# Optimization experiments

Hardware: AMD Instinct MI355X
Metric: run time of the kernel (lower is better)

## Reference

```python
import jax, jax.numpy as jnp
import numpy as np

N = 50000
E = 600000
F_IN = 128
F_OUT = 128


def setup_inputs() -> dict:
    key = jax.random.key(0)
    k = jax.random.split(key, 8)
    x = jax.random.normal(k[0], (N, F_IN), dtype=jnp.float32)
    edge_index = jax.random.randint(k[1], (2, E), 0, N, dtype=jnp.int64)
    edge_weight = jax.random.uniform(k[2], (E,), dtype=jnp.float32)
    # glorot-initialized linear params (w1 is dead code in the original, kept for faithfulness)
    s = float(np.sqrt(6.0 / (F_IN + F_OUT)))
    W1 = jax.random.uniform(k[3], (F_IN, F_OUT), minval=-s, maxval=s, dtype=jnp.float32)
    b1 = jnp.zeros((F_OUT,), dtype=jnp.float32)
    W2 = jax.random.uniform(k[4], (F_IN, F_OUT), minval=-s, maxval=s, dtype=jnp.float32)
    b2 = jnp.zeros((F_OUT,), dtype=jnp.float32)
    a = jnp.full((1,), 0.5, dtype=jnp.float32)
    b = jnp.full((1,), 0.5, dtype=jnp.float32)
    return {"x": x, "edge_index": edge_index, "edge_weight": edge_weight,
            "W1": W1, "b1": b1, "W2": W2, "b2": b2, "a": a, "b": b}


def reference(x, edge_index, edge_weight, W1, b1, W2, b2, a, b):
    # wh_1 = self.w1(x)  (computed but unused in the original forward)
    wh_1 = x @ W1 + b1  # noqa: F841 (dead, DCE'd under jit)
    src, dst = edge_index[0], edge_index[1]
    # gather neighbor features [E, F_IN], scatter-sum to destination nodes [N, F_IN]
    x_j = jax.ops.segment_sum(x[src], dst, num_segments=N)
    wh_2 = x_j @ W2 + b2
    return wh_2
```

## Files before the change

kernel.cpp:

```cpp
#include <hip/hip_runtime.h>

#define F 128
#define CAP 64
#define LDT 136
#define TR 64
#define KC 32
#define LDA 36
#define LDW 160

typedef __attribute__((ext_vector_type(8))) short bf16x8;
typedef __attribute__((ext_vector_type(4))) float f32x4;

__device__ __forceinline__ unsigned short bf16r(float f)
{
    unsigned u = __float_as_uint(f);
    return (unsigned short)((u + 0x7fffu + ((u >> 16) & 1u)) >> 16);
}

__device__ __forceinline__ unsigned pack2(float a, float b)
{
    return (unsigned)bf16r(a) | ((unsigned)bf16r(b) << 16);
}

__device__ __forceinline__ void load_edge(const int* __restrict__ ei, int is64,
                                          int E, int e, int& s, int& d)
{
    if (is64) {
        s = reinterpret_cast<const int2*>(ei)[e].x;
        d = reinterpret_cast<const int2*>(ei)[(size_t)E + e].x;
    } else {
        s = ei[e];
        d = ei[E + e];
    }
}

__device__ __forceinline__ float4 bf16x4_to_f4(uint2 u)
{
    float4 f;
    f.x = __uint_as_float(u.x << 16);
    f.y = __uint_as_float(u.x & 0xffff0000u);
    f.z = __uint_as_float(u.y << 16);
    f.w = __uint_as_float(u.y & 0xffff0000u);
    return f;
}

__device__ __forceinline__ void async_copy16(const void* g, void* lds)
{
    __builtin_amdgcn_global_load_lds(
        (const __attribute__((address_space(1))) unsigned int*)g,
        (__attribute__((address_space(3))) unsigned int*)lds,
        16, 0, 0);
}

__global__ __launch_bounds__(256) void prep_kernel(
    const int* __restrict__ ei, const float* __restrict__ x,
    const float* __restrict__ W, int* __restrict__ flag,
    int* __restrict__ cursor, unsigned int* __restrict__ xh,
    unsigned short* __restrict__ Wt, int N, int M4)
{
    int i = blockIdx.x * 256 + threadIdx.x;
    if (i < M4) {
        float4 v = reinterpret_cast<const float4*>(x)[i];
        uint2 o;
        o.x = pack2(v.x, v.y);
        o.y = pack2(v.z, v.w);
        reinterpret_cast<uint2*>(xh)[i] = o;
    }
    if (i < N) cursor[i] = 0;
    if (i < F * F) {
        int k = i >> 7, n = i & 127;
        Wt[n * F + k] = bf16r(W[i]);
    }
    if (i == 0) {
        int or_hi = ei[1] | ei[3] | ei[5] | ei[7] | ei[9] | ei[11] | ei[13] | ei[15];
        *flag = (or_hi == 0) ? 1 : 0;
    }
}

__global__ __launch_bounds__(256) void position4_kernel(
    const int* __restrict__ ei, const int* __restrict__ flag_p,
    int* __restrict__ cursor, unsigned short* __restrict__ csr16, int E)
{
    const int tid = blockIdx.x * 256 + threadIdx.x;
    const int base = 4 * tid;
    if (base >= E) return;
    const int is64 = *flag_p;

    int s[4], d[4];
    int cnt;
    if (base + 3 < E && (E & 3) == 0) {
        cnt = 4;
        if (is64) {
            const int4* sp = reinterpret_cast<const int4*>(ei);
            int4 a = sp[tid * 2], b = sp[tid * 2 + 1];
            s[0] = a.x; s[1] = a.z; s[2] = b.x; s[3] = b.z;
            const int4* dp = reinterpret_cast<const int4*>(ei) + ((size_t)E >> 1);
            int4 c = dp[tid * 2], e4 = dp[tid * 2 + 1];
            d[0] = c.x; d[1] = c.z; d[2] = e4.x; d[3] = e4.z;
        } else {
            int4 sv = reinterpret_cast<const int4*>(ei)[tid];
            int4 dv = reinterpret_cast<const int4*>(ei + E)[tid];
            s[0] = sv.x; s[1] = sv.y; s[2] = sv.z; s[3] = sv.w;
            d[0] = dv.x; d[1] = dv.y; d[2] = dv.z; d[3] = dv.w;
        }
    } else {
        cnt = E - base; if (cnt > 4) cnt = 4;
        for (int j = 0; j < cnt; ++j) load_edge(ei, is64, E, base + j, s[j], d[j]);
        for (int j = cnt; j < 4; ++j) { s[j] = 0; d[j] = 0; }
    }

    int slot[4];
    #pragma unroll
    for (int j = 0; j < 4; ++j)
        slot[j] = (j < cnt) ? atomicAdd(&cursor[d[j]], 1) : CAP;
    #pragma unroll
    for (int j = 0; j < 4; ++j)
        if (slot[j] < CAP) csr16[(size_t)d[j] * CAP + slot[j]] = (unsigned short)s[j];
}

__global__ __launch_bounds__(256, 8) void gather_async_kernel(
    const unsigned int* __restrict__ xh, const int* __restrict__ ei,
    const int* __restrict__ flag_p, const int* __restrict__ cursor,
    const unsigned short* __restrict__ csr16, unsigned int* __restrict__ aggbf,
    int N, int E)
{
    __shared__ char stg[4][4096];
    const int node = blockIdx.x * 4 + (threadIdx.x >> 6);
    if (node >= N) return;
    const int wv   = threadIdx.x >> 6;
    const int lane = threadIdx.x & 63;
    const int eg   = lane >> 4;
    const int c    = lane & 15;
    char* ldsW = &stg[wv][0];

    const int deg = cursor[node];

    if (deg <= CAP) {
        int sv = (lane < deg) ? (int)csr16[(size_t)node * CAP + lane] : 0;
        float f[8];
        #pragma unroll
        for (int j = 0; j < 8; ++j) f[j] = 0.f;

        for (int ch = 0; ch < deg; ch += 16) {
            int nE = deg - ch; if (nE > 16) nE = 16;
            int nL = (nE + 3) >> 2;
            if (ch > 0) {
                asm volatile("s_waitcnt lgkmcnt(0)" ::: "memory");
                __builtin_amdgcn_sched_barrier(0);
            }
            for (int l = 0; l < nL; ++l) {
                int e = ch + l * 4 + eg;
                int esel = (e < deg) ? e : (deg - 1);
                int src = __shfl(sv, esel);
                async_copy16((const char*)xh + ((size_t)src * 256 + (size_t)c * 16),
                             ldsW + l * 1024);
            }
            asm volatile("s_waitcnt vmcnt(0)" ::: "memory");
            __builtin_amdgcn_sched_barrier(0);
            for (int l = 0; l < nL; ++l) {
                uint4 v = *reinterpret_cast<const uint4*>(ldsW + l * 1024 + lane * 16);
                if (ch + l * 4 + eg < deg) {
                    f[0] += __uint_as_float(v.x << 16);
                    f[1] += __uint_as_float(v.x & 0xffff0000u);
                    f[2] += __uint_as_float(v.y << 16);
                    f[3] += __uint_as_float(v.y & 0xffff0000u);
                    f[4] += __uint_as_float(v.z << 16);
                    f[5] += __uint_as_float(v.z & 0xffff0000u);
                    f[6] += __uint_as_float(v.w << 16);
                    f[7] += __uint_as_float(v.w & 0xffff0000u);
                }
            }
        }
        #pragma unroll
        for (int j = 0; j < 8; ++j) {
            f[j] += __shfl_xor(f[j], 16);
            f[j] += __shfl_xor(f[j], 32);
        }
        if (eg == 0) {
            uint4 o;
            o.x = pack2(f[0], f[1]);
            o.y = pack2(f[2], f[3]);
            o.z = pack2(f[4], f[5]);
            o.w = pack2(f[6], f[7]);
            reinterpret_cast<uint4*>(aggbf)[(size_t)node * 16 + c] = o;
        }
    } else {
        const int half = lane >> 5, col = lane & 31;
        const uint2* x2 = reinterpret_cast<const uint2*>(xh);
        int is64 = *flag_p;
        float4 a0 = make_float4(0.f, 0.f, 0.f, 0.f);
        for (int base = 0; base < E; base += 64) {
            int e = base + lane;
            int s = 0, d = -1;
            if (e < E) load_edge(ei, is64, E, e, s, d);
            unsigned long long m = __ballot(d == node);
            while (m) {
                int i = __ffsll((long long)m) - 1;
                m &= m - 1;
                int sb = __shfl(s, i);
                float4 v = bf16x4_to_f4(x2[(size_t)sb * 32 + col]);
                if (half == 0) { a0.x += v.x; a0.y += v.y; a0.z += v.z; a0.w += v.w; }
            }
        }
        a0.x += __shfl_xor(a0.x, 32);
        a0.y += __shfl_xor(a0.y, 32);
        a0.z += __shfl_xor(a0.z, 32);
        a0.w += __shfl_xor(a0.w, 32);
        if (half == 0) {
            uint2 o;
            o.x = pack2(a0.x, a0.y);
            o.y = pack2(a0.z, a0.w);
            reinterpret_cast<uint2*>(aggbf)[(size_t)node * 32 + col] = o;
        }
    }
}

__global__ __launch_bounds__(256) void gemm_mfma_kernel(
    const unsigned short* __restrict__ aggbf, const unsigned short* __restrict__ Wt,
    const float* __restrict__ bias, float* __restrict__ out, int N)
{
    __shared__ unsigned short sWt[F * LDT];
    const int t = threadIdx.x;

    const uint4* Wg = reinterpret_cast<const uint4*>(Wt);
    #pragma unroll
    for (int u = 0; u < 8; ++u) {
        int idx = u * 256 + t;
        int n = idx >> 4;
        int c = idx & 15;
        *reinterpret_cast<uint4*>(&sWt[n * LDT + c * 8]) = Wg[idx];
    }
    __syncthreads();

    const int wv = t >> 6, lane = t & 63;
    const int quad = lane >> 4, n15 = lane & 15;
    const int rbase = blockIdx.x * 64 + wv * 16;

    f32x4 acc[8];
    #pragma unroll
    for (int i = 0; i < 8; ++i) acc[i] = (f32x4){0.f, 0.f, 0.f, 0.f};

    const int arow = rbase + n15;
    const bool aval = (arow < N);
    #pragma unroll
    for (int kc = 0; kc < F; kc += 32) {
        bf16x8 af;
        if (aval)
            af = *reinterpret_cast<const bf16x8*>(aggbf + (size_t)arow * F + kc + quad * 8);
        else
            af = (bf16x8){0, 0, 0, 0, 0, 0, 0, 0};
        #pragma unroll
        for (int nt = 0; nt < 8; ++nt) {
            bf16x8 bfr = *reinterpret_cast<const bf16x8*>(
                &sWt[(nt * 16 + n15) * LDT + kc + quad * 8]);
            acc[nt] = __builtin_amdgcn_mfma_f32_16x16x32_bf16(af, bfr, acc[nt], 0, 0, 0);
        }
    }

    #pragma unroll
    for (int nt = 0; nt < 8; ++nt) {
        float bv = bias[nt * 16 + n15];
        #pragma unroll
        for (int reg = 0; reg < 4; ++reg) {
            int row = rbase + quad * 4 + reg;
            if (row < N)
                out[(size_t)row * F + nt * 16 + n15] = acc[nt][reg] + bv;
        }
    }
}

__global__ __launch_bounds__(256) void init_kernel(
    const int* __restrict__ ei, int* __restrict__ flag,
    int* __restrict__ zero_arr, int N)
{
    int i = blockIdx.x * 256 + threadIdx.x;
    if (i < N) zero_arr[i] = 0;
    if (i == 0) {
        int or_hi = ei[1] | ei[3] | ei[5] | ei[7] | ei[9] | ei[11] | ei[13] | ei[15];
        *flag = (or_hi == 0) ? 1 : 0;
    }
}

__global__ __launch_bounds__(256) void position_bucket_kernel(
    const int* __restrict__ ei, const int* __restrict__ flag_p,
    int* __restrict__ cursor, int* __restrict__ csr_src, int E)
{
    int e = blockIdx.x * 256 + threadIdx.x;
    if (e >= E) return;
    int s, d;
    load_edge(ei, *flag_p, E, e, s, d);
    int slot = atomicAdd(&cursor[d], 1);
    if (slot < CAP) csr_src[(size_t)d * CAP + slot] = s;
}

__global__ __launch_bounds__(256) void gather_bucket_f32_kernel(
    const float* __restrict__ x, const int* __restrict__ ei,
    const int* __restrict__ flag_p, const int* __restrict__ cursor,
    const int* __restrict__ csr_src, float* __restrict__ agg, int N, int E)
{
    int node = blockIdx.x * 4 + (threadIdx.x >> 6);
    if (node >= N) return;
    int lane = threadIdx.x & 63;
    int half = lane >> 5;
    int col = lane & 31;
    int deg = cursor[node];

    const float4* x4 = reinterpret_cast<const float4*>(x);
    float4 a0 = make_float4(0.f, 0.f, 0.f, 0.f);
    float4 a1 = make_float4(0.f, 0.f, 0.f, 0.f);

    if (deg <= CAP) {
        int sv = (lane < deg) ? csr_src[(size_t)node * CAP + lane] : 0;
        int i = 0;
        for (; i + 3 < deg; i += 4) {
            int e0 = __shfl(sv, i + half);
            int e1 = __shfl(sv, i + 2 + half);
            float4 v0 = x4[(size_t)e0 * 32 + col];
            float4 v1 = x4[(size_t)e1 * 32 + col];
            a0.x += v0.x; a0.y += v0.y; a0.z += v0.z; a0.w += v0.w;
            a1.x += v1.x; a1.y += v1.y; a1.z += v1.z; a1.w += v1.w;
        }
        for (; i + 1 < deg; i += 2) {
            int e0 = __shfl(sv, i + half);
            float4 v0 = x4[(size_t)e0 * 32 + col];
            a0.x += v0.x; a0.y += v0.y; a0.z += v0.z; a0.w += v0.w;
        }
        if (i < deg) {
            int e0 = __shfl(sv, i);
            if (half == 0) {
                float4 v = x4[(size_t)e0 * 32 + col];
                a0.x += v.x; a0.y += v.y; a0.z += v.z; a0.w += v.w;
            }
        }
    } else {
        int is64 = *flag_p;
        for (int base = 0; base < E; base += 64) {
            int e = base + lane;
            int s = 0, d = -1;
            if (e < E) load_edge(ei, is64, E, e, s, d);
            unsigned long long m = __ballot(d == node);
            while (m) {
                int i = __ffsll((long long)m) - 1;
                m &= m - 1;
                int sb = __shfl(s, i);
                float4 v = x4[(size_t)sb * 32 + col];
                if (half == 0) { a0.x += v.x; a0.y += v.y; a0.z += v.z; a0.w += v.w; }
            }
        }
    }
    a0.x += a1.x; a0.y += a1.y; a0.z += a1.z; a0.w += a1.w;
    a0.x += __shfl_xor(a0.x, 32);
    a0.y += __shfl_xor(a0.y, 32);
    a0.z += __shfl_xor(a0.z, 32);
    a0.w += __shfl_xor(a0.w, 32);
    if (half == 0)
        reinterpret_cast<float4*>(agg)[(size_t)node * 32 + col] = a0;
}

__global__ __launch_bounds__(256) void scatter_kernel(
    const float* __restrict__ x, const int* __restrict__ ei,
    const int* __restrict__ flag_p, float* __restrict__ agg, int E)
{
    int tid = blockIdx.x * 256 + threadIdx.x;
    int e = tid >> 5;
    if (e >= E) return;
    int c = (tid & 31) << 2;
    int s, d;
    load_edge(ei, *flag_p, E, e, s, d);
    float4 v = *reinterpret_cast<const float4*>(x + (size_t)s * F + c);
    float* o = agg + (size_t)d * F + c;
    unsafeAtomicAdd(o + 0, v.x);
    unsafeAtomicAdd(o + 1, v.y);
    unsafeAtomicAdd(o + 2, v.z);
    unsafeAtomicAdd(o + 3, v.w);
}

__global__ __launch_bounds__(256) void gemm_kernel(
    float* __restrict__ io, const float* __restrict__ W,
    const float* __restrict__ bias, int N)
{
    __shared__ float sA[TR * LDA];
    __shared__ float sW[KC * LDW];
    const int t = threadIdx.x;
    const int row0 = blockIdx.x * TR;
    const int g = t & 7;
    const int r = t >> 3;

    float acc[2][16];
    #pragma unroll
    for (int i = 0; i < 2; ++i)
        #pragma unroll
        for (int j = 0; j < 16; ++j) acc[i][j] = 0.0f;

    for (int kc = 0; kc < F; kc += KC) {
        #pragma unroll
        for (int u = 0; u < 2; ++u) {
            int idx = u * 256 + t;
            int row = idx >> 3;
            int k4 = (idx & 7) * 4;
            int grow = row0 + row;
            float4 v = (grow < N)
                ? *reinterpret_cast<const float4*>(io + (size_t)grow * F + kc + k4)
                : make_float4(0.f, 0.f, 0.f, 0.f);
            *reinterpret_cast<float4*>(&sA[row * LDA + k4]) = v;
        }
        #pragma unroll
        for (int u = 0; u < 4; ++u) {
            int idx = u * 256 + t;
            int kk = idx >> 5;
            int f4 = (idx & 31) * 4;
            float4 v = *reinterpret_cast<const float4*>(W + (size_t)(kc + kk) * F + f4);
            int chunk = f4 >> 4;
            int within = f4 & 15;
            *reinterpret_cast<float4*>(&sW[kk * LDW + chunk * 20 + within]) = v;
        }
        __syncthreads();

        #pragma unroll 8
        for (int kk = 0; kk < KC; ++kk) {
            const float* wp = &sW[kk * LDW + g * 20];
            const float4 w0 = *reinterpret_cast<const float4*>(wp + 0);
            const float4 w1 = *reinterpret_cast<const float4*>(wp + 4);
            const float4 w2 = *reinterpret_cast<const float4*>(wp + 8);
            const float4 w3 = *reinterpret_cast<const float4*>(wp + 12);
            #pragma unroll
            for (int i = 0; i < 2; ++i) {
                const float xv = sA[(r * 2 + i) * LDA + kk];
                acc[i][0]  += xv * w0.x;  acc[i][1]  += xv * w0.y;
                acc[i][2]  += xv * w0.z;  acc[i][3]  += xv * w0.w;
                acc[i][4]  += xv * w1.x;  acc[i][5]  += xv * w1.y;
                acc[i][6]  += xv * w1.z;  acc[i][7]  += xv * w1.w;
                acc[i][8]  += xv * w2.x;  acc[i][9]  += xv * w2.y;
                acc[i][10] += xv * w2.z;  acc[i][11] += xv * w2.w;
                acc[i][12] += xv * w3.x;  acc[i][13] += xv * w3.y;
                acc[i][14] += xv * w3.z;  acc[i][15] += xv * w3.w;
            }
        }
        __syncthreads();
    }

    float bv[16];
    #pragma unroll
    for (int j = 0; j < 16; ++j) bv[j] = bias[g * 16 + j];
    #pragma unroll
    for (int i = 0; i < 2; ++i) {
        int row = row0 + r * 2 + i;
        if (row < N) {
            float* o = io + (size_t)row * F + g * 16;
            #pragma unroll
            for (int j4 = 0; j4 < 4; ++j4) {
                float4 v;
                v.x = acc[i][j4 * 4 + 0] + bv[j4 * 4 + 0];
                v.y = acc[i][j4 * 4 + 1] + bv[j4 * 4 + 1];
                v.z = acc[i][j4 * 4 + 2] + bv[j4 * 4 + 2];
                v.w = acc[i][j4 * 4 + 3] + bv[j4 * 4 + 3];
                *reinterpret_cast<float4*>(o + j4 * 4) = v;
            }
        }
    }
}

extern "C" void kernel_launch(void* const* d_in, const int* in_sizes, int n_in,
                              void* d_out, int out_size, void* d_ws, size_t ws_size,
                              hipStream_t stream) {
    const float* x  = (const float*)d_in[0];
    const int*   ei = (const int*)d_in[1];
    const float* W2 = (const float*)d_in[5];
    const float* b2 = (const float*)d_in[6];
    float* out = (float*)d_out;

    const int N = in_sizes[0] / F;
    const int E = in_sizes[2];
    const int nblk = (N + 255) / 256;
    const int M = N * (F / 2);
    const int M4 = N * (F / 4);
    const int eblk = (E + 255) / 256;

    int* ws = (int*)d_ws;
    size_t needA = (size_t)16 * 4 + (size_t)N * 4 + (size_t)N * CAP * 2
                 + (size_t)M * 4 + (size_t)F * F * 2 + (size_t)N * (F / 2) * 4;
    size_t needB = (size_t)(16 + N + (size_t)N * CAP) * sizeof(int);

    if (ws_size >= needA && N <= 65536) {
        int* flag    = ws;
        int* cursor  = flag + 16;
        unsigned short* csr16 = (unsigned short*)(cursor + N);
        unsigned int*   xh    = (unsigned int*)(csr16 + (size_t)N * CAP);
        unsigned short* Wt    = (unsigned short*)(xh + M);
        unsigned int*   aggbf = (unsigned int*)(Wt + F * F);

        int pmax = M4; if (N > pmax) pmax = N; if (F * F > pmax) pmax = F * F;
        prep_kernel<<<(pmax + 255) / 256, 256, 0, stream>>>(
            ei, x, W2, flag, cursor, xh, Wt, N, M4);
        int pblk = ((E + 3) / 4 + 255) / 256;
        position4_kernel<<<pblk, 256, 0, stream>>>(ei, flag, cursor, csr16, E);
        gather_async_kernel<<<(N + 3) / 4, 256, 0, stream>>>(
            xh, ei, flag, cursor, csr16, aggbf, N, E);
        gemm_mfma_kernel<<<(N + 63) / 64, 256, 0, stream>>>(
            (const unsigned short*)aggbf, Wt, b2, out, N);
    } else if (ws_size >= needB) {
        int* flag    = ws;
        int* cursor  = flag + 16;
        int* csr_src = cursor + N;
        init_kernel<<<nblk, 256, 0, stream>>>(ei, flag, cursor, N);
        position_bucket_kernel<<<eblk, 256, 0, stream>>>(ei, flag, cursor, csr_src, E);
        gather_bucket_f32_kernel<<<(N + 3) / 4, 256, 0, stream>>>(
            x, ei, flag, cursor, csr_src, out, N, E);
        gemm_kernel<<<(N + TR - 1) / TR, 256, 0, stream>>>(out, W2, b2, N);
    } else {
        int* flag = ws;
        init_kernel<<<1, 64, 0, stream>>>(ei, flag, flag + 16, 0);
        hipMemsetAsync(out, 0, (size_t)N * F * sizeof(float), stream);
        scatter_kernel<<<(E * 32 + 255) / 256, 256, 0, stream>>>(x, ei, flag, out, E);
        gemm_kernel<<<(N + TR - 1) / TR, 256, 0, stream>>>(out, W2, b2, N);
    }
}
```

Measured before the change: 158.4 us.

## Fuse prep, bucketing, gather and GEMM into one cooperative persistent kernel

Replaces the four separate launches (prep, edge bucketing, gather-aggregate, MFMA GEMM) with a single cooperative kernel of 1024 blocks that runs each phase in grid-stride loops separated by grid.sync(). The aim is to remove per-launch overhead and the idle gaps between small kernels. In exchange, every phase is limited to a fixed persistent grid, grid-wide barriers add their own cost, and the gather phase now walks nodes per wave with prefetch instead of a launch sized to N. If the cooperative launch fails, the old multi-kernel path still runs.

```diff
diff --git a/kernel.cpp b/kernel.cpp
--- a/kernel.cpp
+++ b/kernel.cpp
@@ -1,4 +1,7 @@
 #include <hip/hip_runtime.h>
+#include <hip/hip_cooperative_groups.h>
+
+namespace cg = cooperative_groups;
 
 #define F 128
 #define CAP 64
@@ -50,6 +53,223 @@
         (const __attribute__((address_space(1))) unsigned int*)g,
         (__attribute__((address_space(3))) unsigned int*)lds,
         16, 0, 0);
+}
+
+__global__ __launch_bounds__(256, 4) void fused_all_kernel(
+    const float* __restrict__ x, const int* __restrict__ ei,
+    const float* __restrict__ W, const float* __restrict__ bias,
+    float* __restrict__ out, int* __restrict__ cursor,
+    unsigned short* __restrict__ csr16, unsigned int* __restrict__ xh,
+    unsigned short* __restrict__ Wt, unsigned int* __restrict__ aggbf,
+    int N, int E, int M4)
+{
+    __shared__ __align__(16) char smem[F * LDT * 2];
+    cg::grid_group grid = cg::this_grid();
+    const int t   = threadIdx.x;
+    const int tid = blockIdx.x * 256 + t;
+    const int T   = gridDim.x * 256;
+
+    for (int i = tid; i < N; i += T) cursor[i] = 0;
+    for (int i = tid; i < F * F; i += T) {
+        int k = i >> 7, n = i & 127;
+        Wt[n * F + k] = bf16r(W[i]);
+    }
+    grid.sync();
+
+    int or_hi = 0;
+    {
+        int lim = 2 * E; if (lim > 16) lim = 16;
+        for (int j = 1; j < lim; j += 2) or_hi |= ei[j];
+    }
+    const int is64 = (or_hi == 0) ? 1 : 0;
+
+    for (int g4 = tid; g4 * 4 < E; g4 += T) {
+        const int base = g4 * 4;
+        int s[4], d[4], cnt;
+        if (base + 3 < E && (E & 3) == 0) {
+            cnt = 4;
+            if (is64) {
+                const int4* sp = reinterpret_cast<const int4*>(ei);
+                int4 a = sp[g4 * 2], b = sp[g4 * 2 + 1];
+                s[0] = a.x; s[1] = a.z; s[2] = b.x; s[3] = b.z;
+                const int4* dp = reinterpret_cast<const int4*>(ei) + ((size_t)E >> 1);
+                int4 c4 = dp[g4 * 2], e4 = dp[g4 * 2 + 1];
+                d[0] = c4.x; d[1] = c4.z; d[2] = e4.x; d[3] = e4.z;
+            } else {
+                int4 sv4 = reinterpret_cast<const int4*>(ei)[g4];
+                int4 dv4 = reinterpret_cast<const int4*>(ei + E)[g4];
+                s[0] = sv4.x; s[1] = sv4.y; s[2] = sv4.z; s[3] = sv4.w;
+                d[0] = dv4.x; d[1] = dv4.y; d[2] = dv4.z; d[3] = dv4.w;
+            }
+        } else {
+            cnt = E - base; if (cnt > 4) cnt = 4;
+            for (int j = 0; j < cnt; ++j) load_edge(ei, is64, E, base + j, s[j], d[j]);
+            for (int j = cnt; j < 4; ++j) { s[j] = 0; d[j] = 0; }
+            goto tail;
+        }
+        cnt = 4;
+    tail:
+        int slot[4];
+        #pragma unroll
+        for (int j = 0; j < 4; ++j)
+            slot[j] = (j < cnt) ? atomicAdd(&cursor[d[j]], 1) : CAP;
+        #pragma unroll
+        for (int j = 0; j < 4; ++j)
+            if (slot[j] < CAP) csr16[(size_t)d[j] * CAP + slot[j]] = (unsigned short)s[j];
+    }
+    for (int i = tid; i < M4; i += T) {
+        float4 v = reinterpret_cast<const float4*>(x)[i];
+        uint2 o;
+        o.x = pack2(v.x, v.y);
+        o.y = pack2(v.z, v.w);
+        reinterpret_cast<uint2*>(xh)[i] = o;
+    }
+    grid.sync();
+
+    const int wv = t >> 6, lane = t & 63;
+    const int eg = lane >> 4;
+    const int c  = lane & 15;
+    char* ldsW = smem + wv * 4096;
+    const int wid   = blockIdx.x * 4 + wv;
+    const int wstep = gridDim.x * 4;
+
+    int node = wid;
+    int deg = 0, sv = 0;
+    if (node < N) {
+        deg = cursor[node];
+        sv  = (int)csr16[(size_t)node * CAP + lane];
+    }
+    while (node < N) {
+        const int nnode = node + wstep;
+        int ndeg = 0, nsv = 0;
+        if (nnode < N) {
+            ndeg = cursor[nnode];
+            nsv  = (int)csr16[(size_t)nnode * CAP + lane];
+        }
+        if (deg <= CAP) {
+            float f[8];
+            #pragma unroll
+            for (int j = 0; j < 8; ++j) f[j] = 0.f;
+            for (int ch = 0; ch < deg; ch += 16) {
+                int nE = deg - ch; if (nE > 16) nE = 16;
+                int nL = (nE + 3) >> 2;
+                asm volatile("s_waitcnt lgkmcnt(0)" ::: "memory");
+                __builtin_amdgcn_sched_barrier(0);
+                for (int l = 0; l < nL; ++l) {
+                    int e = ch + l * 4 + eg;
+                    int esel = (e < deg) ? e : (deg - 1);
+                    int src = __shfl(sv, esel);
+                    async_copy16((const char*)xh + ((size_t)src * 256 + (size_t)c * 16),
+                                 ldsW + l * 1024);
+                }
+                asm volatile("s_waitcnt vmcnt(0)" ::: "memory");
+                __builtin_amdgcn_sched_barrier(0);
+                for (int l = 0; l < nL; ++l) {
+                    uint4 v = *reinterpret_cast<const uint4*>(ldsW + l * 1024 + lane * 16);
+                    if (ch + l * 4 + eg < deg) {
+                        f[0] += __uint_as_float(v.x << 16);
+                        f[1] += __uint_as_float(v.x & 0xffff0000u);
+                        f[2] += __uint_as_float(v.y << 16);
+                        f[3] += __uint_as_float(v.y & 0xffff0000u);
+                        f[4] += __uint_as_float(v.z << 16);
+                        f[5] += __uint_as_float(v.z & 0xffff0000u);
+                        f[6] += __uint_as_float(v.w << 16);
+                        f[7] += __uint_as_float(v.w & 0xffff0000u);
+                    }
+                }
+            }
+            #pragma unroll
+            for (int j = 0; j < 8; ++j) {
+                f[j] += __shfl_xor(f[j], 16);
+                f[j] += __shfl_xor(f[j], 32);
+            }
+            if (eg == 0) {
+                uint4 o;
+                o.x = pack2(f[0], f[1]);
+                o.y = pack2(f[2], f[3]);
+                o.z = pack2(f[4], f[5]);
+                o.w = pack2(f[6], f[7]);
+                reinterpret_cast<uint4*>(aggbf)[(size_t)node * 16 + c] = o;
+            }
+        } else {
+            const int half = lane >> 5, col = lane & 31;
+            const uint2* x2 = reinterpret_cast<const uint2*>(xh);
+            float4 a0 = make_float4(0.f, 0.f, 0.f, 0.f);
+            for (int base = 0; base < E; base += 64) {
+                int e = base + lane;
+                int ss = 0, dd = -1;
+                if (e < E) load_edge(ei, is64, E, e, ss, dd);
+                unsigned long long m = __ballot(dd == node);
+                while (m) {
+                    int i = __ffsll((long long)m) - 1;
+                    m &= m - 1;
+                    int sb = __shfl(ss, i);
+                    float4 v = bf16x4_to_f4(x2[(size_t)sb * 32 + col]);
+                    if (half == 0) { a0.x += v.x; a0.y += v.y; a0.z += v.z; a0.w += v.w; }
+                }
+            }
+            a0.x += __shfl_xor(a0.x, 32);
+            a0.y += __shfl_xor(a0.y, 32);
+            a0.z += __shfl_xor(a0.z, 32);
+            a0.w += __shfl_xor(a0.w, 32);
+            if (half == 0) {
+                uint2 o;
+                o.x = pack2(a0.x, a0.y);
+                o.y = pack2(a0.z, a0.w);
+                reinterpret_cast<uint2*>(aggbf)[(size_t)node * 32 + col] = o;
+            }
+        }
+        node = nnode; deg = ndeg; sv = nsv;
+    }
+    grid.sync();
+
+    unsigned short* sWt = (unsigned short*)smem;
+    const uint4* Wg = reinterpret_cast<const uint4*>(Wt);
+    #pragma unroll
+    for (int u = 0; u < 8; ++u) {
+        int idx = u * 256 + t;
+        int n = idx >> 4;
+        int cc = idx & 15;
+        *reinterpret_cast<uint4*>(&sWt[n * LDT + cc * 8]) = Wg[idx];
+    }
+    __syncthreads();
+
+    const int quad = lane >> 4, n15 = lane & 15;
+    const unsigned short* agg16 = (const unsigned short*)aggbf;
+    for (int tile = blockIdx.x; tile * 64 < N; tile += gridDim.x) {
+        const int rbase = tile * 64 + wv * 16;
+        f32x4 acc[8];
+        #pragma unroll
+        for (int i = 0; i < 8; ++i) acc[i] = (f32x4){0.f, 0.f, 0.f, 0.f};
+
+        const int arow = rbase + n15;
+        const bool aval = (arow < N);
+        #pragma unroll
+        for (int kc = 0; kc < F; kc += 32) {
+            bf16x8 af;
+            if (aval)
+                af = *reinterpret_cast<const bf16x8*>(agg16 + (size_t)arow * F + kc + quad * 8);
+            else
+                af = (bf16x8){0, 0, 0, 0, 0, 0, 0, 0};
+            #pragma unroll
+            for (int nt = 0; nt < 8; ++nt) {
+                bf16x8 bfr = *reinterpret_cast<const bf16x8*>(
+                    &sWt[(nt * 16 + n15) * LDT + kc + quad * 8]);
+                acc[nt] = __builtin_amdgcn_mfma_f32_16x16x32_bf16(af, bfr, acc[nt], 0, 0, 0);
+            }
+        }
+
+        #pragma unroll
+        for (int nt = 0; nt < 8; ++nt) {
+            float bv = bias[nt * 16 + n15];
+            #pragma unroll
+            for (int reg = 0; reg < 4; ++reg) {
+                int row = rbase + quad * 4 + reg;
+                if (row < N)
+                    out[(size_t)row * F + nt * 16 + n15] = acc[nt][reg] + bv;
+            }
+        }
+    }
 }
 
 __global__ __launch_bounds__(256) void prep_kernel(
@@ -488,6 +708,16 @@
         unsigned int*   xh    = (unsigned int*)(csr16 + (size_t)N * CAP);
         unsigned short* Wt    = (unsigned short*)(xh + M);
         unsigned int*   aggbf = (unsigned int*)(Wt + F * F);
+
+        int Nv = N, Ev = E, M4v = M4;
+        void* args[] = {
+            (void*)&x, (void*)&ei, (void*)&W2, (void*)&b2, (void*)&out,
+            (void*)&cursor, (void*)&csr16, (void*)&xh, (void*)&Wt, (void*)&aggbf,
+            (void*)&Nv, (void*)&Ev, (void*)&M4v
+        };
+        hipError_t cerr = hipLaunchCooperativeKernel(
+            (const void*)fused_all_kernel, dim3(1024), dim3(256), args, 0, stream);
+        if (cerr == hipSuccess) return;
 
         int pmax = M4; if (N > pmax) pmax = N; if (F * F > pmax) pmax = F * F;
         prep_kernel<<<(pmax + 255) / 256, 256, 0, stream>>>(
```

Result: slower. 514.1 us (+224.6%).
